# Kernel tuning notes

Measured on AMD Instinct MI355X. Metric: run time of the kernel, lower is better.

Reference implementation:

```python
import jax, jax.numpy as jnp
import numpy as np

N_NODES = 50000
N_EDGES = 800000
IN_F = 64
OUT_F = 64
N_REL = 32
N_BASES = 30


def setup_inputs() -> dict:
    key = jax.random.key(0)
    ks = jax.random.split(key, 6)
    x = jax.random.normal(ks[0], (N_NODES, IN_F), dtype=jnp.float32)
    edge_index = jax.random.randint(ks[1], (2, N_EDGES), 0, N_NODES, dtype=jnp.int64)
    edge_type = jax.random.randint(ks[2], (N_EDGES,), 0, N_REL, dtype=jnp.int64)
    basis = jax.random.normal(ks[3], (N_BASES, IN_F, OUT_F), dtype=jnp.float32) * 0.01
    coeff = jax.random.normal(ks[4], (N_REL, N_BASES), dtype=jnp.float32) * 0.01
    self_weight = jax.random.normal(ks[5], (IN_F, OUT_F), dtype=jnp.float32) * 0.01
    bias = jnp.zeros((OUT_F,), dtype=jnp.float32)
    return {"x": x, "edge_index": edge_index, "edge_type": edge_type,
            "num_nodes": N_NODES, "basis": basis, "coeff": coeff,
            "self_weight": self_weight, "bias": bias}


def reference(x, edge_index, edge_type, num_nodes, basis, coeff, self_weight, bias):
    # W_r = sum_b coeff[r,b] * basis[b]  -> (R, in, out)
    rel_weight = jnp.einsum('rb,bio->rio', coeff, basis)
    source_idx = edge_index[0]
    target_idx = edge_index[1]
    src_feats = x[source_idx]  # (E, in)

    def body(out, rw_r):
        rw, r = rw_r
        mask = (edge_type == r).astype(jnp.float32)  # (E,)
        msg = (src_feats @ rw) * mask[:, None]       # (E, out)
        return out.at[target_idx].add(msg), None

    out0 = jnp.zeros((num_nodes, rel_weight.shape[-1]), dtype=jnp.float32)
    out, _ = jax.lax.scan(body, out0, (rel_weight, jnp.arange(rel_weight.shape[0])))

    in_degree = jnp.zeros((num_nodes,), dtype=jnp.float32).at[target_idx].add(1.0)
    in_degree = jnp.maximum(in_degree, 1.0)
    out = out / in_degree[:, None]
    out = out + x @ self_weight + bias
    return out
```

## Files before the change

kernel.cpp:

```cpp
#include <hip/hip_runtime.h>
#include <hip/hip_bf16.h>

#define IN_F   64
#define OUT_F  64
#define N_RELS 32
#define N_BAS  30
#define KROW   2048
#define B1CHUNK 8192
#define ESTCAP 2048

typedef __attribute__((ext_vector_type(8))) short short8v;
typedef __attribute__((ext_vector_type(8))) _Float16 half8v;
typedef __attribute__((ext_vector_type(4))) float f32x4;

__device__ __forceinline__ int dmin(int a, int b) { return a < b ? a : b; }
__device__ __forceinline__ unsigned short f2bf(float f) {
    __hip_bfloat16 h = __float2bfloat16(f);
    return *(unsigned short*)&h;
}

__global__ void k_bbt(const float* __restrict__ basis, const float* __restrict__ sw,
                      const float* __restrict__ bias, __hip_bfloat16* __restrict__ bbT) {
    int idx = blockIdx.x * blockDim.x + threadIdx.x;
    if (idx >= OUT_F * KROW) return;
    int e = idx & 7, lane = (idx >> 3) & 63, s = (idx >> 9) & 15, kq = (idx >> 13) & 3, cb = idx >> 15;
    int l15 = lane & 15, lk = lane >> 4;
    int o = cb * 16 + l15;
    int k = kq * 512 + s * 32 + lk * 8 + e;
    int i = k >> 5, b = k & 31;
    float v;
    if (b < N_BAS)      v = basis[((size_t)b * IN_F + i) * OUT_F + o];
    else if (b == 30)   v = sw[(size_t)i * OUT_F + o];
    else                v = (i == 0) ? bias[o] : 0.f;
    bbT[idx] = __float2bfloat16(v);
}

__global__ void k_xpack(const float* __restrict__ x, unsigned* __restrict__ xh, int N) {
    int idx = blockIdx.x * blockDim.x + threadIdx.x;
    if (idx >= N * 32) return;
    int g = idx & 31, n = idx >> 5;
    int f = (g & 15) + ((g >> 4) << 5);
    _Float16 lo = (_Float16)x[((size_t)n << 6) + f];
    _Float16 hi = (_Float16)x[((size_t)n << 6) + f + 16];
    xh[idx] = (unsigned)*(unsigned short*)&lo | ((unsigned)*(unsigned short*)&hi << 16);
}

__global__ void __launch_bounds__(256)
k_b1a(const int* __restrict__ tgt, int* __restrict__ gsum, int E) {
    __shared__ int lh[256];
    int tid = threadIdx.x;
    lh[tid] = 0;
    __syncthreads();
    for (int i = blockIdx.x * blockDim.x + tid; i < E; i += gridDim.x * blockDim.x)
        atomicAdd(&lh[tgt[i] >> 8], 1);
    __syncthreads();
    if (lh[tid]) atomicAdd(&gsum[tid], lh[tid]);
}

__global__ void k_scanB(const int* __restrict__ gsum, int* __restrict__ gexcl,
                        int* __restrict__ bcur, int* __restrict__ off, int NB, int N) {
    int l = threadIdx.x;
    int a0 = (4*l+0 < NB) ? gsum[4*l+0] : 0;
    int a1 = (4*l+1 < NB) ? gsum[4*l+1] : 0;
    int a2 = (4*l+2 < NB) ? gsum[4*l+2] : 0;
    int a3 = (4*l+3 < NB) ? gsum[4*l+3] : 0;
    int s = a0 + a1 + a2 + a3;
    int sc = s;
    for (int d = 1; d < 64; d <<= 1) {
        int o = __shfl_up(sc, d, 64);
        if (l >= d) sc += o;
    }
    int base = sc - s;
    if (4*l+0 < NB) { gexcl[4*l+0] = base;          bcur[4*l+0] = base; }
    if (4*l+1 < NB) { gexcl[4*l+1] = base+a0;       bcur[4*l+1] = base+a0; }
    if (4*l+2 < NB) { gexcl[4*l+2] = base+a0+a1;    bcur[4*l+2] = base+a0+a1; }
    if (4*l+3 < NB) { gexcl[4*l+3] = base+a0+a1+a2; bcur[4*l+3] = base+a0+a1+a2; }
    if (l == 63) { gexcl[NB] = sc; off[N] = sc; }
}

__global__ void __launch_bounds__(1024)
k_b1(const int* __restrict__ src, const int* __restrict__ tgt, const int* __restrict__ et,
     int* __restrict__ bcur, unsigned* __restrict__ ssr, int E) {
    __shared__ unsigned ls_p[B1CHUNK];
    __shared__ unsigned char ls_b[B1CHUNK];
    __shared__ int lh[256], lbase[256], gbase[256], lcur[256];
    int tid = threadIdx.x;
    int e0 = blockIdx.x * B1CHUNK;
    int n = E - e0; if (n > B1CHUNK) n = B1CHUNK;
    if (tid < 256) { lh[tid] = 0; lcur[tid] = 0; }
    __syncthreads();
    unsigned pr[8]; int br[8];
#pragma unroll
    for (int k = 0; k < 8; ++k) {
        int i = k * 1024 + tid;
        br[k] = -1;
        if (i < n) {
            int t = tgt[e0 + i];
            br[k] = t >> 8;
            pr[k] = ((unsigned)(t & 255) << 21) | ((unsigned)src[e0 + i] << 5) | (unsigned)et[e0 + i];
            atomicAdd(&lh[br[k]], 1);
        }
    }
    __syncthreads();
    if (tid < 64) {
        int a0 = lh[4*tid], a1 = lh[4*tid+1], a2 = lh[4*tid+2], a3 = lh[4*tid+3];
        int s = a0 + a1 + a2 + a3, sc = s;
        for (int d = 1; d < 64; d <<= 1) {
            int o = __shfl_up(sc, d, 64);
            if (tid >= d) sc += o;
        }
        int base = sc - s;
        lbase[4*tid] = base; lbase[4*tid+1] = base+a0;
        lbase[4*tid+2] = base+a0+a1; lbase[4*tid+3] = base+a0+a1+a2;
    }
    __syncthreads();
    if (tid < 256 && lh[tid]) gbase[tid] = atomicAdd(&bcur[tid], lh[tid]);
    __syncthreads();
#pragma unroll
    for (int k = 0; k < 8; ++k) {
        if (br[k] >= 0) {
            int pos = atomicAdd(&lcur[br[k]], 1);
            int s = lbase[br[k]] + pos;
            ls_p[s] = pr[k];
            ls_b[s] = (unsigned char)br[k];
        }
    }
    __syncthreads();
#pragma unroll
    for (int k = 0; k < 8; ++k) {
        int i = k * 1024 + tid;
        if (i < n) {
            int b = ls_b[i];
            ssr[gbase[b] + (i - lbase[b])] = ls_p[i];
        }
    }
}

__global__ void __launch_bounds__(256)
k_b2(const unsigned* __restrict__ ssr, const int* __restrict__ gexcl,
     int* __restrict__ off, unsigned* __restrict__ ssr2, int N) {
    __shared__ int lh[256], lofs[256], lcur[256];
    int g = blockIdx.x, tid = threadIdx.x;
    int o0 = gexcl[g], o1 = gexcl[g + 1];
    lh[tid] = 0;
    __syncthreads();
    for (int i = o0 + tid; i < o1; i += 256)
        atomicAdd(&lh[ssr[i] >> 21], 1);
    __syncthreads();
    if (tid < 64) {
        int a0 = lh[4*tid], a1 = lh[4*tid+1], a2 = lh[4*tid+2], a3 = lh[4*tid+3];
        int s = a0 + a1 + a2 + a3, sc = s;
        for (int d = 1; d < 64; d <<= 1) {
            int o = __shfl_up(sc, d, 64);
            if (tid >= d) sc += o;
        }
        int base = sc - s;
        lofs[4*tid] = base; lofs[4*tid+1] = base+a0;
        lofs[4*tid+2] = base+a0+a1; lofs[4*tid+3] = base+a0+a1+a2;
    }
    __syncthreads();
    int t = (g << 8) + tid;
    if (t < N) off[t] = o0 + lofs[tid];
    lcur[tid] = o0 + lofs[tid];
    __syncthreads();
    for (int i = o0 + tid; i < o1; i += 256) {
        unsigned p = ssr[i];
        int pos = atomicAdd(&lcur[p >> 21], 1);
        ssr2[pos] = p;
    }
}

__global__ void __launch_bounds__(1024, 8)
k_fused(const float* __restrict__ x, const unsigned* __restrict__ xh,
        const unsigned* __restrict__ ssr2, const int* __restrict__ off,
        const float* __restrict__ coeff, const __hip_bfloat16* __restrict__ bbT,
        float* __restrict__ out, int N) {
    __shared__ __align__(16) unsigned char zb[16 * 4096];
    __shared__ __align__(16) float pf[16 * 256];
    unsigned* cofs2 = (unsigned*)pf;
    unsigned* est   = ((unsigned*)pf) + 640;
    int tid = threadIdx.x;
    int w = tid >> 6, lane = tid & 63;
    int mh = w & 1;
    int t0 = blockIdx.x * 16;

    int tA = t0 + (w >> 1), tB = tA + 8;
    int okA = (tA < N), okB = (tB < N);
    int offA0 = okA ? off[tA] : 0;
    int offA1 = okA ? off[tA + 1] : 0;
    int offB0 = okB ? off[tB] : 0;
    int offB1 = okB ? off[tB + 1] : 0;
    float xsA = okA ? x[((size_t)tA << 6) + (mh << 5) + (lane & 31)] : 0.f;
    float xsB = okB ? x[((size_t)tB << 6) + (mh << 5) + (lane & 31)] : 0.f;

    int bs0 = off[t0];
    int bse = off[dmin(t0 + 16, N)];
    int stage_n = dmin(bse - bs0, ESTCAP);

    for (int idx = tid; idx < 33 * 16; idx += 1024) {
        int r = idx >> 4, c = idx & 15;
        float lo = (r < 32) ? coeff[r * N_BAS + c] : 0.f;
        float hi = (r < 32 && (c + 16) < N_BAS) ? coeff[r * N_BAS + c + 16] : 0.f;
        _Float16 hl = (_Float16)lo, hh = (_Float16)hi;
        cofs2[idx] = (unsigned)*(unsigned short*)&hl | ((unsigned)*(unsigned short*)&hh << 16);
    }
    for (int i = tid; i < stage_n; i += 1024)
        est[i] = ssr2[bs0 + i];
    __syncthreads();

    int l15 = lane & 15, lk = lane >> 4;
    int vq = lk << 3;
    int vperm = (lane & 48) << 1;
    unsigned xadd2 = (unsigned)(((mh << 4) + l15) << 2);
    const char* xhB = (const char*)xh;

    auto do_round = [&](int tIdx, int s0r, int s1r, float xselfv) {
        int deg = s1r - s0r;
        f32x4 acc00 = {0.f,0.f,0.f,0.f};
        f32x4 acc01 = acc00, acc10 = acc00, acc11 = acc00;
        if (deg > 0) {
            int last = s1r - 1;
            int locLast = last - bs0;
            bool staged = (locLast < stage_n);
#pragma unroll 1
            for (int kt = 0; kt * 32 < deg; ++kt) {
                int rem = deg - kt * 32;
                unsigned wjv[8];
                if (staged) {
                    int locb = (s0r - bs0) + kt * 32 + vq;
#pragma unroll
                    for (int j = 0; j < 8; ++j)
                        wjv[j] = est[dmin(locb + j, locLast)];
                } else {
                    unsigned ew = ssr2[dmin(s0r + kt * 32 + (lane & 31), last)];
#pragma unroll
                    for (int j = 0; j < 8; ++j)
                        wjv[j] = (unsigned)__builtin_amdgcn_ds_bpermute(vperm + j * 4, (int)ew);
                }
                union { unsigned short u[8]; half8v h; } bf0, bf1, a0, a1;
#pragma unroll
                for (int j = 0; j < 8; ++j) {
                    unsigned wj = wjv[j];
                    unsigned rrow = ((vq + j) < rem) ? (wj & 31u) : 32u;
                    unsigned bw = cofs2[(rrow << 4) + l15];
                    unsigned xw = *(const unsigned*)(xhB + (((size_t)((wj >> 5) & 0xFFFFu)) << 7) + xadd2);
                    bf0.u[j] = (unsigned short)(bw & 0xFFFFu);
                    bf1.u[j] = (unsigned short)(bw >> 16);
                    a0.u[j]  = (unsigned short)(xw & 0xFFFFu);
                    a1.u[j]  = (unsigned short)(xw >> 16);
                }
                acc00 = __builtin_amdgcn_mfma_f32_16x16x32_f16(a0.h, bf0.h, acc00, 0, 0, 0);
                acc01 = __builtin_amdgcn_mfma_f32_16x16x32_f16(a0.h, bf1.h, acc01, 0, 0, 0);
                acc10 = __builtin_amdgcn_mfma_f32_16x16x32_f16(a1.h, bf0.h, acc10, 0, 0, 0);
                acc11 = __builtin_amdgcn_mfma_f32_16x16x32_f16(a1.h, bf1.h, acc11, 0, 0, 0);
            }
        }
        float inv = 1.f / fmaxf((float)deg, 1.f);
        unsigned rb = (unsigned)tIdx << 12;
        unsigned swz = (unsigned)((tIdx & 7) << 4);
#pragma unroll
        for (int q = 0; q < 4; ++q) {
            int i0 = (mh << 5) + (lk << 2) + q;
            int i1 = i0 + 16;
            *(unsigned short*)(zb + rb + ((((unsigned)i0 << 6) + ((unsigned)l15 << 1)) ^ swz))        = f2bf(acc00[q] * inv);
            *(unsigned short*)(zb + rb + ((((unsigned)i0 << 6) + ((unsigned)(16 + l15) << 1)) ^ swz)) = f2bf(acc01[q] * inv);
            *(unsigned short*)(zb + rb + ((((unsigned)i1 << 6) + ((unsigned)l15 << 1)) ^ swz))        = f2bf(acc10[q] * inv);
            *(unsigned short*)(zb + rb + ((((unsigned)i1 << 6) + ((unsigned)(16 + l15) << 1)) ^ swz)) = f2bf(acc11[q] * inv);
        }
        if (lane < 32) {
            unsigned by = (((unsigned)(((mh << 5) + lane) << 6)) + 60u) ^ swz;
            *(unsigned short*)(zb + rb + by) = f2bf(xselfv);
            if (mh == 0 && lane == 0)
                *(unsigned short*)(zb + rb + (62u ^ swz)) = (unsigned short)0x3F80;
        }
    };

    do_round((w >> 1),     offA0, offA1, xsA);
    do_round((w >> 1) + 8, offB0, offB1, xsB);
    __syncthreads();

    {
        int colblk = w & 3, kq = w >> 2;
        const char* bp2 = (const char*)bbT + (((unsigned)(colblk * 4 + kq)) << 14) + ((unsigned)lane << 4);
        unsigned arow = (unsigned)l15 << 12;
        unsigned aswz = (unsigned)((l15 & 7) << 4);
        f32x4 acc2 = {0.f,0.f,0.f,0.f};
#pragma unroll 4
        for (int s = 0; s < 16; ++s) {
            unsigned abyte = ((unsigned)((kq << 10) + (s << 6) + (lk << 4))) ^ aswz;
            short8v a = *(const short8v*)(zb + arow + abyte);
            short8v b = *(const short8v*)(bp2 + (s << 10));
            acc2 = __builtin_amdgcn_mfma_f32_16x16x32_bf16(a, b, acc2, 0, 0, 0);
        }
#pragma unroll
        for (int q = 0; q < 4; ++q)
            pf[(w << 8) + ((lk << 2) + q) * 16 + l15] = acc2[q];
    }
    __syncthreads();

    {
        int row = w, col = lane;
        int cb = col >> 4, cl = col & 15;
        int tt = t0 + row;
        if (tt < N) {
            float v = pf[(((0 << 2) + cb) << 8) + (row << 4) + cl]
                    + pf[(((1 << 2) + cb) << 8) + (row << 4) + cl]
                    + pf[(((2 << 2) + cb) << 8) + (row << 4) + cl]
                    + pf[(((3 << 2) + cb) << 8) + (row << 4) + cl];
            out[((size_t)tt << 6) + col] = v;
        }
    }
}

extern "C" void kernel_launch(void* const* d_in, const int* in_sizes, int n_in,
                              void* d_out, int out_size, void* d_ws, size_t ws_size,
                              hipStream_t stream) {
    const float* x     = (const float*)d_in[0];
    const int*   eidx  = (const int*)d_in[1];
    const int*   etype = (const int*)d_in[2];
    const float* basis = (const float*)d_in[4];
    const float* coeff = (const float*)d_in[5];
    const float* sw    = (const float*)d_in[6];
    const float* bias  = (const float*)d_in[7];

    const int E = in_sizes[1] / 2;
    const int N = out_size / OUT_F;
    const int NB = (N + 255) >> 8;
    const int* srcv = eidx;
    const int* tgtv = eidx + E;
    float* out = (float*)d_out;

    size_t p = 0;
    auto alloc = [&](size_t bytes) { size_t cur = p; p += (bytes + 255) & ~(size_t)255; return cur; };
    char* base = (char*)d_ws;
    __hip_bfloat16* bbT   = (__hip_bfloat16*)(base + alloc((size_t)OUT_F * KROW * 2));
    int*            gsum  = (int*)(base + alloc(256 * 4));
    int*            gexcl = (int*)(base + alloc((size_t)(NB + 1) * 4));
    int*            bcur  = (int*)(base + alloc((size_t)NB * 4));
    int*            off   = (int*)(base + alloc((size_t)(N + 1) * 4));
    unsigned*       ssr   = (unsigned*)(base + alloc((size_t)E * 4));
    unsigned*       ssr2  = (unsigned*)(base + alloc((size_t)E * 4));
    unsigned*       xh    = (unsigned*)(base + alloc((size_t)N * 32 * 4));
    (void)ws_size;

    hipMemsetAsync(gsum, 0, 256 * 4, stream);

    k_bbt<<<(OUT_F * KROW + 255) / 256, 256, 0, stream>>>(basis, sw, bias, bbT);
    k_xpack<<<(N * 32 + 255) / 256, 256, 0, stream>>>(x, xh, N);
    k_b1a<<<256, 256, 0, stream>>>(tgtv, gsum, E);
    k_scanB<<<1, 64, 0, stream>>>(gsum, gexcl, bcur, off, NB, N);
    k_b1<<<(E + B1CHUNK - 1) / B1CHUNK, 1024, 0, stream>>>(srcv, tgtv, etype, bcur, ssr, E);
    k_b2<<<NB, 256, 0, stream>>>(ssr, gexcl, off, ssr2, N);
    k_fused<<<(N + 15) / 16, 1024, 0, stream>>>(x, xh, ssr2, off, coeff, bbT, out, N);
}
```

Baseline: 129.7 us.

## Prefetch first edge tile into registers before barrier; retune binning kernel sizes

The fused kernel no longer stages each block's edge list into shared memory. Each wave instead loads its first 32 edges and their packed source features into registers before the block barrier, so those global loads overlap the coefficient setup and the sync. Later tiles still use bpermute from global. The binning kernels are retuned: k_b1 uses 2048-edge chunks with 256 threads, k_b2 uses 1024 threads, and k_b1a gets more blocks. This adds more small blocks and more global atomics on the bucket cursors in k_b1, and raises register pressure in the fused kernel.

```diff
diff --git a/kernel.cpp b/kernel.cpp
--- a/kernel.cpp
+++ b/kernel.cpp
@@ -6,8 +6,7 @@
 #define N_RELS 32
 #define N_BAS  30
 #define KROW   2048
-#define B1CHUNK 8192
-#define ESTCAP 2048
+#define B1CHUNK 2048
 
 typedef __attribute__((ext_vector_type(8))) short short8v;
 typedef __attribute__((ext_vector_type(8))) _Float16 half8v;
@@ -78,7 +77,7 @@
     if (l == 63) { gexcl[NB] = sc; off[N] = sc; }
 }
 
-__global__ void __launch_bounds__(1024)
+__global__ void __launch_bounds__(256)
 k_b1(const int* __restrict__ src, const int* __restrict__ tgt, const int* __restrict__ et,
      int* __restrict__ bcur, unsigned* __restrict__ ssr, int E) {
     __shared__ unsigned ls_p[B1CHUNK];
@@ -87,12 +86,12 @@
     int tid = threadIdx.x;
     int e0 = blockIdx.x * B1CHUNK;
     int n = E - e0; if (n > B1CHUNK) n = B1CHUNK;
-    if (tid < 256) { lh[tid] = 0; lcur[tid] = 0; }
+    lh[tid] = 0; lcur[tid] = 0;
     __syncthreads();
     unsigned pr[8]; int br[8];
 #pragma unroll
     for (int k = 0; k < 8; ++k) {
-        int i = k * 1024 + tid;
+        int i = k * 256 + tid;
         br[k] = -1;
         if (i < n) {
             int t = tgt[e0 + i];
@@ -114,7 +113,7 @@
         lbase[4*tid+2] = base+a0+a1; lbase[4*tid+3] = base+a0+a1+a2;
     }
     __syncthreads();
-    if (tid < 256 && lh[tid]) gbase[tid] = atomicAdd(&bcur[tid], lh[tid]);
+    if (lh[tid]) gbase[tid] = atomicAdd(&bcur[tid], lh[tid]);
     __syncthreads();
 #pragma unroll
     for (int k = 0; k < 8; ++k) {
@@ -128,7 +127,7 @@
     __syncthreads();
 #pragma unroll
     for (int k = 0; k < 8; ++k) {
-        int i = k * 1024 + tid;
+        int i = k * 256 + tid;
         if (i < n) {
             int b = ls_b[i];
             ssr[gbase[b] + (i - lbase[b])] = ls_p[i];
@@ -136,15 +135,15 @@
     }
 }
 
-__global__ void __launch_bounds__(256)
+__global__ void __launch_bounds__(1024)
 k_b2(const unsigned* __restrict__ ssr, const int* __restrict__ gexcl,
      int* __restrict__ off, unsigned* __restrict__ ssr2, int N) {
     __shared__ int lh[256], lofs[256], lcur[256];
     int g = blockIdx.x, tid = threadIdx.x;
     int o0 = gexcl[g], o1 = gexcl[g + 1];
-    lh[tid] = 0;
-    __syncthreads();
-    for (int i = o0 + tid; i < o1; i += 256)
+    if (tid < 256) lh[tid] = 0;
+    __syncthreads();
+    for (int i = o0 + tid; i < o1; i += 1024)
         atomicAdd(&lh[ssr[i] >> 21], 1);
     __syncthreads();
     if (tid < 64) {
@@ -159,11 +158,13 @@
         lofs[4*tid+2] = base+a0+a1; lofs[4*tid+3] = base+a0+a1+a2;
     }
     __syncthreads();
-    int t = (g << 8) + tid;
-    if (t < N) off[t] = o0 + lofs[tid];
-    lcur[tid] = o0 + lofs[tid];
-    __syncthreads();
-    for (int i = o0 + tid; i < o1; i += 256) {
+    if (tid < 256) {
+        int t = (g << 8) + tid;
+        if (t < N) off[t] = o0 + lofs[tid];
+        lcur[tid] = o0 + lofs[tid];
+    }
+    __syncthreads();
+    for (int i = o0 + tid; i < o1; i += 1024) {
         unsigned p = ssr[i];
         int pos = atomicAdd(&lcur[p >> 21], 1);
         ssr2[pos] = p;
@@ -178,7 +179,6 @@
     __shared__ __align__(16) unsigned char zb[16 * 4096];
     __shared__ __align__(16) float pf[16 * 256];
     unsigned* cofs2 = (unsigned*)pf;
-    unsigned* est   = ((unsigned*)pf) + 640;
     int tid = threadIdx.x;
     int w = tid >> 6, lane = tid & 63;
     int mh = w & 1;
@@ -193,9 +193,38 @@
     float xsA = okA ? x[((size_t)tA << 6) + (mh << 5) + (lane & 31)] : 0.f;
     float xsB = okB ? x[((size_t)tB << 6) + (mh << 5) + (lane & 31)] : 0.f;
 
-    int bs0 = off[t0];
-    int bse = off[dmin(t0 + 16, N)];
-    int stage_n = dmin(bse - bs0, ESTCAP);
+    int l15 = lane & 15, lk = lane >> 4;
+    int vq = lk << 3;
+    int vperm = (lane & 48) << 1;
+    unsigned xadd2 = (unsigned)(((mh << 4) + l15) << 2);
+    const char* xhB = (const char*)xh;
+
+    int s0A = __builtin_amdgcn_readfirstlane(offA0);
+    int s1A = __builtin_amdgcn_readfirstlane(offA1);
+    int s0B = __builtin_amdgcn_readfirstlane(offB0);
+    int s1B = __builtin_amdgcn_readfirstlane(offB1);
+
+    unsigned wA[8], xA[8], wB[8], xB[8];
+    if (s1A > s0A) {
+        int last = s1A - 1;
+        unsigned ew = ssr2[dmin(s0A + (lane & 31), last)];
+#pragma unroll
+        for (int j = 0; j < 8; ++j)
+            wA[j] = (unsigned)__builtin_amdgcn_ds_bpermute(vperm + j * 4, (int)ew);
+#pragma unroll
+        for (int j = 0; j < 8; ++j)
+            xA[j] = *(const unsigned*)(xhB + (((size_t)((wA[j] >> 5) & 0xFFFFu)) << 7) + xadd2);
+    }
+    if (s1B > s0B) {
+        int last = s1B - 1;
+        unsigned ew = ssr2[dmin(s0B + (lane & 31), last)];
+#pragma unroll
+        for (int j = 0; j < 8; ++j)
+            wB[j] = (unsigned)__builtin_amdgcn_ds_bpermute(vperm + j * 4, (int)ew);
+#pragma unroll
+        for (int j = 0; j < 8; ++j)
+            xB[j] = *(const unsigned*)(xhB + (((size_t)((wB[j] >> 5) & 0xFFFFu)) << 7) + xadd2);
+    }
 
     for (int idx = tid; idx < 33 * 16; idx += 1024) {
         int r = idx >> 4, c = idx & 15;
@@ -204,43 +233,41 @@
         _Float16 hl = (_Float16)lo, hh = (_Float16)hi;
         cofs2[idx] = (unsigned)*(unsigned short*)&hl | ((unsigned)*(unsigned short*)&hh << 16);
     }
-    for (int i = tid; i < stage_n; i += 1024)
-        est[i] = ssr2[bs0 + i];
-    __syncthreads();
-
-    int l15 = lane & 15, lk = lane >> 4;
-    int vq = lk << 3;
-    int vperm = (lane & 48) << 1;
-    unsigned xadd2 = (unsigned)(((mh << 4) + l15) << 2);
-    const char* xhB = (const char*)xh;
-
-    auto do_round = [&](int tIdx, int s0r, int s1r, float xselfv) {
+    __syncthreads();
+
+    auto compute = [&](int tIdx, int s0r, int s1r, float xselfv,
+                       unsigned (&wv)[8], unsigned (&xv)[8]) {
         int deg = s1r - s0r;
         f32x4 acc00 = {0.f,0.f,0.f,0.f};
         f32x4 acc01 = acc00, acc10 = acc00, acc11 = acc00;
         if (deg > 0) {
             int last = s1r - 1;
-            int locLast = last - bs0;
-            bool staged = (locLast < stage_n);
+            {
+                union { unsigned short u[8]; half8v h; } bf0, bf1, a0, a1;
+#pragma unroll
+                for (int j = 0; j < 8; ++j) {
+                    unsigned wj = wv[j];
+                    unsigned rrow = ((vq + j) < deg) ? (wj & 31u) : 32u;
+                    unsigned bw = cofs2[(rrow << 4) + l15];
+                    unsigned xw = xv[j];
+                    bf0.u[j] = (unsigned short)(bw & 0xFFFFu);
+                    bf1.u[j] = (unsigned short)(bw >> 16);
+                    a0.u[j]  = (unsigned short)(xw & 0xFFFFu);
+                    a1.u[j]  = (unsigned short)(xw >> 16);
+                }
+                acc00 = __builtin_amdgcn_mfma_f32_16x16x32_f16(a0.h, bf0.h, acc00, 0, 0, 0);
+                acc01 = __builtin_amdgcn_mfma_f32_16x16x32_f16(a0.h, bf1.h, acc01, 0, 0, 0);
+                acc10 = __builtin_amdgcn_mfma_f32_16x16x32_f16(a1.h, bf0.h, acc10, 0, 0, 0);
+                acc11 = __builtin_amdgcn_mfma_f32_16x16x32_f16(a1.h, bf1.h, acc11, 0, 0, 0);
+            }
 #pragma unroll 1
-            for (int kt = 0; kt * 32 < deg; ++kt) {
+            for (int kt = 1; kt * 32 < deg; ++kt) {
                 int rem = deg - kt * 32;
-                unsigned wjv[8];
-                if (staged) {
-                    int locb = (s0r - bs0) + kt * 32 + vq;
-#pragma unroll
-                    for (int j = 0; j < 8; ++j)
-                        wjv[j] = est[dmin(locb + j, locLast)];
-                } else {
-                    unsigned ew = ssr2[dmin(s0r + kt * 32 + (lane & 31), last)];
-#pragma unroll
-                    for (int j = 0; j < 8; ++j)
-                        wjv[j] = (unsigned)__builtin_amdgcn_ds_bpermute(vperm + j * 4, (int)ew);
-                }
+                unsigned ew = ssr2[dmin(s0r + kt * 32 + (lane & 31), last)];
                 union { unsigned short u[8]; half8v h; } bf0, bf1, a0, a1;
 #pragma unroll
                 for (int j = 0; j < 8; ++j) {
-                    unsigned wj = wjv[j];
+                    unsigned wj = (unsigned)__builtin_amdgcn_ds_bpermute(vperm + j * 4, (int)ew);
                     unsigned rrow = ((vq + j) < rem) ? (wj & 31u) : 32u;
                     unsigned bw = cofs2[(rrow << 4) + l15];
                     unsigned xw = *(const unsigned*)(xhB + (((size_t)((wj >> 5) & 0xFFFFu)) << 7) + xadd2);
@@ -275,8 +302,8 @@
         }
     };
 
-    do_round((w >> 1),     offA0, offA1, xsA);
-    do_round((w >> 1) + 8, offB0, offB1, xsB);
+    compute((w >> 1),     s0A, s1A, xsA, wA, xA);
+    compute((w >> 1) + 8, s0B, s1B, xsB, wB, xB);
     __syncthreads();
 
     {
@@ -347,9 +374,9 @@
 
     k_bbt<<<(OUT_F * KROW + 255) / 256, 256, 0, stream>>>(basis, sw, bias, bbT);
     k_xpack<<<(N * 32 + 255) / 256, 256, 0, stream>>>(x, xh, N);
-    k_b1a<<<256, 256, 0, stream>>>(tgtv, gsum, E);
+    k_b1a<<<512, 256, 0, stream>>>(tgtv, gsum, E);
     k_scanB<<<1, 64, 0, stream>>>(gsum, gexcl, bcur, off, NB, N);
-    k_b1<<<(E + B1CHUNK - 1) / B1CHUNK, 1024, 0, stream>>>(srcv, tgtv, etype, bcur, ssr, E);
-    k_b2<<<NB, 256, 0, stream>>>(ssr, gexcl, off, ssr2, N);
+    k_b1<<<(E + B1CHUNK - 1) / B1CHUNK, 256, 0, stream>>>(srcv, tgtv, etype, bcur, ssr, E);
+    k_b2<<<NB, 1024, 0, stream>>>(ssr, gexcl, off, ssr2, N);
     k_fused<<<(N + 15) / 16, 1024, 0, stream>>>(x, xh, ssr2, off, coeff, bbT, out, N);
 }
```

Result: slower. 146.2 us (+12.7%).

## Stage per-target edge lists in fixed LDS slots and transpose zb layout

Applied to the files above, without the earlier changes.

Replaces the block-wide contiguous edge staging with per-target 128-entry LDS slots filled by each wave, so staged edge words can be read with two 16-byte vector loads instead of eight clamped scalar reads. Reorders the basis/K dimension to basis-major (k = b*64+i), letting each lane pack four bf16 results into one 8-byte LDS store, and adds a second XOR swizzle term to avoid bank conflicts. Duplicates the coefficient table in LDS so half-waves hit separate copies, and uses readfirstlane to keep edge offsets scalar. Targets with more than 128 edges fall back to the global path, and the new layout must stay consistent between bbT and the second-stage reads.

```diff
diff --git a/kernel.cpp b/kernel.cpp
--- a/kernel.cpp
+++ b/kernel.cpp
@@ -7,11 +7,12 @@
 #define N_BAS  30
 #define KROW   2048
 #define B1CHUNK 8192
-#define ESTCAP 2048
 
 typedef __attribute__((ext_vector_type(8))) short short8v;
 typedef __attribute__((ext_vector_type(8))) _Float16 half8v;
 typedef __attribute__((ext_vector_type(4))) float f32x4;
+typedef __attribute__((ext_vector_type(4))) unsigned u32x4;
+typedef __attribute__((ext_vector_type(2))) unsigned u32x2;
 
 __device__ __forceinline__ int dmin(int a, int b) { return a < b ? a : b; }
 __device__ __forceinline__ unsigned short f2bf(float f) {
@@ -27,7 +28,7 @@
     int l15 = lane & 15, lk = lane >> 4;
     int o = cb * 16 + l15;
     int k = kq * 512 + s * 32 + lk * 8 + e;
-    int i = k >> 5, b = k & 31;
+    int b = k >> 6, i = k & 63;
     float v;
     if (b < N_BAS)      v = basis[((size_t)b * IN_F + i) * OUT_F + o];
     else if (b == 30)   v = sw[(size_t)i * OUT_F + o];
@@ -178,7 +179,7 @@
     __shared__ __align__(16) unsigned char zb[16 * 4096];
     __shared__ __align__(16) float pf[16 * 256];
     unsigned* cofs2 = (unsigned*)pf;
-    unsigned* est   = ((unsigned*)pf) + 640;
+    unsigned* est   = ((unsigned*)pf) + 1120;
     int tid = threadIdx.x;
     int w = tid >> 6, lane = tid & 63;
     int mh = w & 1;
@@ -193,19 +194,30 @@
     float xsA = okA ? x[((size_t)tA << 6) + (mh << 5) + (lane & 31)] : 0.f;
     float xsB = okB ? x[((size_t)tB << 6) + (mh << 5) + (lane & 31)] : 0.f;
 
-    int bs0 = off[t0];
-    int bse = off[dmin(t0 + 16, N)];
-    int stage_n = dmin(bse - bs0, ESTCAP);
+    int s0A = __builtin_amdgcn_readfirstlane(offA0);
+    int s1A = __builtin_amdgcn_readfirstlane(offA1);
+    int s0B = __builtin_amdgcn_readfirstlane(offB0);
+    int s1B = __builtin_amdgcn_readfirstlane(offB1);
 
     for (int idx = tid; idx < 33 * 16; idx += 1024) {
         int r = idx >> 4, c = idx & 15;
         float lo = (r < 32) ? coeff[r * N_BAS + c] : 0.f;
         float hi = (r < 32 && (c + 16) < N_BAS) ? coeff[r * N_BAS + c + 16] : 0.f;
         _Float16 hl = (_Float16)lo, hh = (_Float16)hi;
-        cofs2[idx] = (unsigned)*(unsigned short*)&hl | ((unsigned)*(unsigned short*)&hh << 16);
-    }
-    for (int i = tid; i < stage_n; i += 1024)
-        est[i] = ssr2[bs0 + i];
+        unsigned v = (unsigned)*(unsigned short*)&hl | ((unsigned)*(unsigned short*)&hh << 16);
+        cofs2[idx] = v;
+        cofs2[idx + 560] = v;
+    }
+    {
+        int sgt = mh ? s0B : s0A;
+        int sg1 = mh ? s1B : s1A;
+        int slot = (w >> 1) + (mh << 3);
+        int degS = sg1 - sgt;
+        if (degS > 0 && degS <= 128) {
+            if (lane < degS)      est[slot * 128 + lane]      = ssr2[sgt + lane];
+            if (lane + 64 < degS) est[slot * 128 + lane + 64] = ssr2[sgt + lane + 64];
+        }
+    }
     __syncthreads();
 
     int l15 = lane & 15, lk = lane >> 4;
@@ -213,24 +225,25 @@
     int vperm = (lane & 48) << 1;
     unsigned xadd2 = (unsigned)(((mh << 4) + l15) << 2);
     const char* xhB = (const char*)xh;
-
-    auto do_round = [&](int tIdx, int s0r, int s1r, float xselfv) {
+    unsigned cbase = (unsigned)((lk & 1) * 560);
+
+    auto compute = [&](int tIdx, int s0r, int s1r, float xselfv) {
         int deg = s1r - s0r;
         f32x4 acc00 = {0.f,0.f,0.f,0.f};
         f32x4 acc01 = acc00, acc10 = acc00, acc11 = acc00;
         if (deg > 0) {
             int last = s1r - 1;
-            int locLast = last - bs0;
-            bool staged = (locLast < stage_n);
+            bool staged = (deg <= 128);
 #pragma unroll 1
             for (int kt = 0; kt * 32 < deg; ++kt) {
                 int rem = deg - kt * 32;
                 unsigned wjv[8];
                 if (staged) {
-                    int locb = (s0r - bs0) + kt * 32 + vq;
-#pragma unroll
-                    for (int j = 0; j < 8; ++j)
-                        wjv[j] = est[dmin(locb + j, locLast)];
+                    const unsigned char* ep = (const unsigned char*)(est + tIdx * 128 + kt * 32 + vq);
+                    u32x4 w0 = *(const u32x4*)ep;
+                    u32x4 w1 = *(const u32x4*)(ep + 16);
+                    wjv[0] = w0[0]; wjv[1] = w0[1]; wjv[2] = w0[2]; wjv[3] = w0[3];
+                    wjv[4] = w1[0]; wjv[5] = w1[1]; wjv[6] = w1[2]; wjv[7] = w1[3];
                 } else {
                     unsigned ew = ssr2[dmin(s0r + kt * 32 + (lane & 31), last)];
 #pragma unroll
@@ -241,9 +254,11 @@
 #pragma unroll
                 for (int j = 0; j < 8; ++j) {
                     unsigned wj = wjv[j];
-                    unsigned rrow = ((vq + j) < rem) ? (wj & 31u) : 32u;
-                    unsigned bw = cofs2[(rrow << 4) + l15];
-                    unsigned xw = *(const unsigned*)(xhB + (((size_t)((wj >> 5) & 0xFFFFu)) << 7) + xadd2);
+                    bool okj = (vq + j) < rem;
+                    unsigned rrow = okj ? (wj & 31u) : 32u;
+                    unsigned wjs  = okj ? wj : 0u;
+                    unsigned bw = cofs2[cbase + (rrow << 4) + l15];
+                    unsigned xw = *(const unsigned*)(xhB + (((size_t)((wjs >> 5) & 0xFFFFu)) << 7) + xadd2);
                     bf0.u[j] = (unsigned short)(bw & 0xFFFFu);
                     bf1.u[j] = (unsigned short)(bw >> 16);
                     a0.u[j]  = (unsigned short)(xw & 0xFFFFu);
@@ -258,25 +273,45 @@
         float inv = 1.f / fmaxf((float)deg, 1.f);
         unsigned rb = (unsigned)tIdx << 12;
         unsigned swz = (unsigned)((tIdx & 7) << 4);
-#pragma unroll
-        for (int q = 0; q < 4; ++q) {
-            int i0 = (mh << 5) + (lk << 2) + q;
-            int i1 = i0 + 16;
-            *(unsigned short*)(zb + rb + ((((unsigned)i0 << 6) + ((unsigned)l15 << 1)) ^ swz))        = f2bf(acc00[q] * inv);
-            *(unsigned short*)(zb + rb + ((((unsigned)i0 << 6) + ((unsigned)(16 + l15) << 1)) ^ swz)) = f2bf(acc01[q] * inv);
-            *(unsigned short*)(zb + rb + ((((unsigned)i1 << 6) + ((unsigned)l15 << 1)) ^ swz))        = f2bf(acc10[q] * inv);
-            *(unsigned short*)(zb + rb + ((((unsigned)i1 << 6) + ((unsigned)(16 + l15) << 1)) ^ swz)) = f2bf(acc11[q] * inv);
+        unsigned ib = (unsigned)((mh << 5) + (lk << 2));
+        {
+            unsigned short h0, h1, h2, h3;
+            u32x2 pv;
+            h0 = f2bf(acc00[0]*inv); h1 = f2bf(acc00[1]*inv); h2 = f2bf(acc00[2]*inv); h3 = f2bf(acc00[3]*inv);
+            pv[0] = h0 | ((unsigned)h1 << 16); pv[1] = h2 | ((unsigned)h3 << 16);
+            unsigned byt = ((unsigned)l15 << 7) + (ib << 1);
+            byt ^= swz ^ (((byt >> 7) & 7) << 4);
+            *(u32x2*)(zb + rb + byt) = pv;
+            h0 = f2bf(acc01[0]*inv); h1 = f2bf(acc01[1]*inv); h2 = f2bf(acc01[2]*inv); h3 = f2bf(acc01[3]*inv);
+            pv[0] = h0 | ((unsigned)h1 << 16); pv[1] = h2 | ((unsigned)h3 << 16);
+            byt = ((unsigned)(16 + l15) << 7) + (ib << 1);
+            byt ^= swz ^ (((byt >> 7) & 7) << 4);
+            *(u32x2*)(zb + rb + byt) = pv;
+            h0 = f2bf(acc10[0]*inv); h1 = f2bf(acc10[1]*inv); h2 = f2bf(acc10[2]*inv); h3 = f2bf(acc10[3]*inv);
+            pv[0] = h0 | ((unsigned)h1 << 16); pv[1] = h2 | ((unsigned)h3 << 16);
+            byt = ((unsigned)l15 << 7) + ((ib + 16) << 1);
+            byt ^= swz ^ (((byt >> 7) & 7) << 4);
+            *(u32x2*)(zb + rb + byt) = pv;
+            h0 = f2bf(acc11[0]*inv); h1 = f2bf(acc11[1]*inv); h2 = f2bf(acc11[2]*inv); h3 = f2bf(acc11[3]*inv);
+            pv[0] = h0 | ((unsigned)h1 << 16); pv[1] = h2 | ((unsigned)h3 << 16);
+            byt = ((unsigned)(16 + l15) << 7) + ((ib + 16) << 1);
+            byt ^= swz ^ (((byt >> 7) & 7) << 4);
+            *(u32x2*)(zb + rb + byt) = pv;
         }
         if (lane < 32) {
-            unsigned by = (((unsigned)(((mh << 5) + lane) << 6)) + 60u) ^ swz;
-            *(unsigned short*)(zb + rb + by) = f2bf(xselfv);
-            if (mh == 0 && lane == 0)
-                *(unsigned short*)(zb + rb + (62u ^ swz)) = (unsigned short)0x3F80;
+            unsigned byt = (30u << 7) + ((unsigned)((mh << 5) + lane) << 1);
+            byt ^= swz ^ (((byt >> 7) & 7) << 4);
+            *(unsigned short*)(zb + rb + byt) = f2bf(xselfv);
+            if (mh == 0 && lane == 0) {
+                unsigned byb = (31u << 7);
+                byb ^= swz ^ (((byb >> 7) & 7) << 4);
+                *(unsigned short*)(zb + rb + byb) = (unsigned short)0x3F80;
+            }
         }
     };
 
-    do_round((w >> 1),     offA0, offA1, xsA);
-    do_round((w >> 1) + 8, offB0, offB1, xsB);
+    compute((w >> 1),     s0A, s1A, xsA);
+    compute((w >> 1) + 8, s0B, s1B, xsB);
     __syncthreads();
 
     {
@@ -287,7 +322,8 @@
         f32x4 acc2 = {0.f,0.f,0.f,0.f};
 #pragma unroll 4
         for (int s = 0; s < 16; ++s) {
-            unsigned abyte = ((unsigned)((kq << 10) + (s << 6) + (lk << 4))) ^ aswz;
+            unsigned abyte = (unsigned)((kq << 10) + (s << 6) + (lk << 4));
+            abyte ^= aswz ^ (((abyte >> 7) & 7) << 4);
             short8v a = *(const short8v*)(zb + arow + abyte);
             short8v b = *(const short8v*)(bp2 + (s << 10));
             acc2 = __builtin_amdgcn_mfma_f32_16x16x32_bf16(a, b, acc2, 0, 0, 0);
```

After: 139.7 us. 7.8% more time.
